# Kernel optimization log

Measured on AMD Instinct MI355X. Metric: run time of the kernel, lower is better.

Reference implementation:

```python
import jax, jax.numpy as jnp
import numpy as np
import math

B, H, T, N = 2, 4, 2048, 2048
THETA = 2.0 ** 16


def get_freqs(n: int, theta: float) -> jnp.ndarray:
    # quantize arange to multiples of 2, matching torch (t/2).floor()*2
    t = jnp.arange(n, dtype=jnp.float32)
    q = jnp.floor(t / 2.0) * 2.0
    return 1.0 / theta ** (q / n) / (2.0 * math.pi)


def rope(phases: jnp.ndarray, v: jnp.ndarray) -> jnp.ndarray:
    # v: [B,H,T,N]; phases: [T,N] (broadcast). Interleaved pair rotation.
    ph = (phases % 1.0) * (2.0 * math.pi)
    c, s = jnp.cos(ph), jnp.sin(ph)
    v2 = v.reshape(*v.shape[:-1], -1, 2)           # [...,N/2,2]
    v_rot = jnp.stack((-v2[..., 1], v2[..., 0]), axis=-1).reshape(v.shape)
    return (v * c + v_rot * s).astype(v.dtype)


def setup_inputs() -> dict:
    key = jax.random.key(0)
    kq, kv = jax.random.split(key)
    Q = jax.random.normal(kq, (B, H, T, N), dtype=jnp.float32)
    V = jax.random.normal(kv, (B, H, T, N), dtype=jnp.float32)
    return {"Q": Q, "V": V}


def reference(Q, V):
    Tlen = Q.shape[2]
    n = Q.shape[3]
    freqs = get_freqs(n, THETA)                               # [N]
    phases = jnp.arange(Tlen, dtype=jnp.float32)[:, None] * freqs[None, :]  # [T,N]
    QR = rope(phases, Q)                                      # K is Q -> KR = QR
    scores = jnp.einsum('bhtn,bhsn->bhts', QR, QR)            # [B,H,T,T]
    # strictly-causal mask: keep s < t (tril with diagonal=-1)
    mask = jnp.tril(jnp.ones((Tlen, Tlen), dtype=bool), k=-1)
    scores = jnp.where(mask, scores, 0.0)
    out = jnp.einsum('bhts,bhsn->bhtn', scores, V)
    return out
```

## Files before the change

kernel.cpp:

```cpp
#include <hip/hip_runtime.h>
#include <hip/hip_bf16.h>

#define TDIM 2048
#define NDIM 2048
#define BHN  8
#define LD   2048

typedef __attribute__((ext_vector_type(8))) short bf16x8;
typedef __attribute__((ext_vector_type(4))) float f32x4;
typedef unsigned short us;

static __device__ __forceinline__ us f2bf(float x) {
  union { __hip_bfloat16 h; us u; } cv;
  cv.h = __float2bfloat16(x);
  return cv.u;
}

__global__ __launch_bounds__(256) void rope_kernel(const float* __restrict__ Q,
                                                   us* __restrict__ QR,
                                                   int total8) {
  int idx = blockIdx.x * blockDim.x + threadIdx.x;
  if (idx >= total8) return;
  long base = (long)idx * 8;
  int n = (int)(base & (NDIM - 1));
  int t = (int)((base >> 11) & (TDIM - 1));
  const float4* p = reinterpret_cast<const float4*>(Q + base);
  float4 v0 = p[0], v1 = p[1];
  float q[8] = {v0.x, v0.y, v0.z, v0.w, v1.x, v1.y, v1.z, v1.w};
  us r[8];
  float tf = (float)t;
#pragma unroll
  for (int pr = 0; pr < 4; ++pr) {
    int nn = n + pr * 2;
    float freq = __builtin_exp2f((float)nn * (-1.0f / 128.0f)) * 0.15915494309189535f;
    float ph = tf * freq;
    ph = ph - __builtin_floorf(ph);
    float c = __builtin_amdgcn_cosf(ph);
    float s = __builtin_amdgcn_sinf(ph);
    float e = q[2 * pr], o = q[2 * pr + 1];
    r[2 * pr]     = f2bf(e * c - o * s);
    r[2 * pr + 1] = f2bf(o * c + e * s);
  }
  union { us usv[8]; bf16x8 v; } pk;
#pragma unroll
  for (int i = 0; i < 8; ++i) pk.usv[i] = r[i];
  *reinterpret_cast<bf16x8*>(QR + base) = pk.v;
}

__global__ __launch_bounds__(256) void vtrans_kernel(const float* __restrict__ V,
                                                     us* __restrict__ VT,
                                                     us* __restrict__ Sflag) {
  __shared__ float tile[32][33];
  if (Sflag != nullptr && blockIdx.x == 0 && blockIdx.y == 0 && blockIdx.z == 0 &&
      threadIdx.x == 0 && threadIdx.y == 0) {
    for (int h = 0; h < BHN; ++h) {
      unsigned* f = (unsigned*)(Sflag + (long)h * TDIM * LD + 1792);
      for (int i = 0; i < 40; ++i)
        __hip_atomic_store(&f[i], 0u, __ATOMIC_RELAXED, __HIP_MEMORY_SCOPE_AGENT);
    }
  }
  int bh = blockIdx.z;
  int n0 = blockIdx.x * 32, t0 = blockIdx.y * 32;
  const float* Vp = V + (long)bh * TDIM * NDIM;
  us* Tp = VT + (long)bh * TDIM * NDIM;
  int tx = threadIdx.x, ty = threadIdx.y;
#pragma unroll
  for (int i = 0; i < 4; ++i)
    tile[ty + i * 8][tx] = Vp[(long)(t0 + ty + i * 8) * NDIM + n0 + tx];
  __syncthreads();
#pragma unroll
  for (int i = 0; i < 4; ++i)
    Tp[(long)(n0 + ty + i * 8) * TDIM + t0 + tx] = f2bf(tile[tx][ty + i * 8]);
}

template <int PASS>
__device__ __forceinline__ void run_tile(const us* __restrict__ A,
                                         const us* __restrict__ B,
                                         void* __restrict__ Cbase,
                                         us* __restrict__ lds,
                                         int rt, int ct, int tid,
                                         unsigned* __restrict__ fh) {
  const int lane = tid & 63, wid = tid >> 6;
  const int wr = wid >> 2, wc = wid & 3;
  const int l15 = lane & 15, l4 = lane >> 4;
  const int row0 = rt * 256, col0 = ct * 256;
  const int kts = (PASS == 0) ? 32 : (rt + 1) * 4;
  const int fbase = rt * (rt + 1) / 2;

  if constexpr (PASS == 1) {
    if (wid == 0) {
      unsigned need = (1u << (rt + 1)) - 1u;
      for (;;) {
        unsigned ok = 0;
        if (lane <= rt)
          ok = (__hip_atomic_fetch_add(&fh[fbase + lane], 0u, __ATOMIC_RELAXED,
                                       __HIP_MEMORY_SCOPE_AGENT) != 0u);
        unsigned long long m = __ballot(ok);
        if (((unsigned)m & need) == need) break;
        __builtin_amdgcn_s_sleep(8);
      }
    }
    __builtin_amdgcn_s_barrier();
    asm volatile("" ::: "memory");
  }

  f32x4 acc[8][4];
#pragma unroll
  for (int m = 0; m < 8; ++m)
#pragma unroll
    for (int n = 0; n < 4; ++n) acc[m][n] = (f32x4){0.f, 0.f, 0.f, 0.f};

  auto stage = [&](int half , int t) {
    const us* g0 = (half < 2) ? A : B;
    const int tr0 = (half < 2) ? row0 : col0;
    const int h = half & 1;
    us* lb = lds + ((half < 2) ? 0 : 32768) + (t & 1) * 16384;
    const int k0 = t * 64;
#pragma unroll
    for (int r = 0; r < 2; ++r) {
      int off = r * 512 + tid;
      int row = off >> 3;
      int ch = off & 7;
      int chl = ch ^ (row & 7);
      const us* g = g0 + (long)(tr0 + h * 128 + row) * LD + (k0 + chl * 8);
      us* l = lb + h * 8192 + off * 8;
      __builtin_amdgcn_global_load_lds(
          (const __attribute__((address_space(1))) unsigned int*)g,
          (__attribute__((address_space(3))) unsigned int*)l, 16, 0, 0);
    }
  };
  auto ldA = [&](int b, int m, int ks) -> bf16x8 {
    int row = wr * 128 + m * 16 + l15;
    int ch = (ks * 4 + l4) ^ (row & 7);
    return *reinterpret_cast<const bf16x8*>(lds + b * 16384 + row * 64 + ch * 8);
  };
  auto ldB = [&](int b, int n, int ks) -> bf16x8 {
    int row = wc * 64 + n * 16 + l15;
    int ch = (ks * 4 + l4) ^ (row & 7);
    return *reinterpret_cast<const bf16x8*>(lds + 32768 + b * 16384 + row * 64 + ch * 8);
  };

  stage(0, 0); stage(1, 0); stage(2, 0); stage(3, 0);
  if (1 < kts) { stage(2, 1); stage(3, 1); }
  asm volatile("s_waitcnt vmcnt(4)" ::: "memory");
  __builtin_amdgcn_s_barrier();
  __builtin_amdgcn_sched_barrier(0);

  bf16x8 af[4][2], bfr[4][2];
  for (int t = 0; t < kts; ++t) {
    const int b = t & 1;
#pragma unroll
    for (int m = 0; m < 4; ++m) { af[m][0] = ldA(b, m, 0); af[m][1] = ldA(b, m, 1); }
#pragma unroll
    for (int n = 0; n < 2; ++n) { bfr[n][0] = ldB(b, n, 0); bfr[n][1] = ldB(b, n, 1); }
    if (t + 1 < kts) stage(0, t + 1);
    __builtin_amdgcn_s_barrier();
    asm volatile("s_waitcnt lgkmcnt(0)" ::: "memory");
    __builtin_amdgcn_sched_barrier(0);
    __builtin_amdgcn_s_setprio(1);
#pragma unroll
    for (int m = 0; m < 4; ++m)
#pragma unroll
      for (int n = 0; n < 2; ++n)
#pragma unroll
        for (int ks = 0; ks < 2; ++ks)
          acc[m][n] = __builtin_amdgcn_mfma_f32_16x16x32_bf16(af[m][ks], bfr[n][ks], acc[m][n], 0, 0, 0);
    __builtin_amdgcn_s_setprio(0);
    __builtin_amdgcn_sched_barrier(0);
    __builtin_amdgcn_s_barrier();
#pragma unroll
    for (int n = 2; n < 4; ++n) { bfr[n][0] = ldB(b, n, 0); bfr[n][1] = ldB(b, n, 1); }
    if (t + 1 < kts) stage(1, t + 1);
    __builtin_amdgcn_s_barrier();
    asm volatile("s_waitcnt lgkmcnt(0)" ::: "memory");
    __builtin_amdgcn_sched_barrier(0);
    __builtin_amdgcn_s_setprio(1);
#pragma unroll
    for (int m = 0; m < 4; ++m)
#pragma unroll
      for (int n = 2; n < 4; ++n)
#pragma unroll
        for (int ks = 0; ks < 2; ++ks)
          acc[m][n] = __builtin_amdgcn_mfma_f32_16x16x32_bf16(af[m][ks], bfr[n][ks], acc[m][n], 0, 0, 0);
    __builtin_amdgcn_s_setprio(0);
    __builtin_amdgcn_sched_barrier(0);
    __builtin_amdgcn_s_barrier();
#pragma unroll
    for (int m = 0; m < 4; ++m) { af[m][0] = ldA(b, m + 4, 0); af[m][1] = ldA(b, m + 4, 1); }
    if (t + 2 < kts) stage(2, t + 2);
    __builtin_amdgcn_s_barrier();
    asm volatile("s_waitcnt lgkmcnt(0)" ::: "memory");
    __builtin_amdgcn_sched_barrier(0);
    __builtin_amdgcn_s_setprio(1);
#pragma unroll
    for (int m = 0; m < 4; ++m)
#pragma unroll
      for (int n = 0; n < 2; ++n)
#pragma unroll
        for (int ks = 0; ks < 2; ++ks)
          acc[m + 4][n] = __builtin_amdgcn_mfma_f32_16x16x32_bf16(af[m][ks], bfr[n][ks], acc[m + 4][n], 0, 0, 0);
    __builtin_amdgcn_s_setprio(0);
    __builtin_amdgcn_sched_barrier(0);
    __builtin_amdgcn_s_barrier();
    if (t + 2 < kts) stage(3, t + 2);
    __builtin_amdgcn_s_setprio(1);
#pragma unroll
    for (int m = 0; m < 4; ++m)
#pragma unroll
      for (int n = 2; n < 4; ++n)
#pragma unroll
        for (int ks = 0; ks < 2; ++ks)
          acc[m + 4][n] = __builtin_amdgcn_mfma_f32_16x16x32_bf16(af[m][ks], bfr[n][ks], acc[m + 4][n], 0, 0, 0);
    __builtin_amdgcn_s_setprio(0);
    if (t + 2 < kts) { asm volatile("s_waitcnt vmcnt(4)" ::: "memory"); }
    else             { asm volatile("s_waitcnt vmcnt(0)" ::: "memory"); }
    __builtin_amdgcn_sched_barrier(0);
    __builtin_amdgcn_s_barrier();
    __builtin_amdgcn_sched_barrier(0);
  }

  if constexpr (PASS == 0) {
    us* C = (us*)Cbase;
    const bool diag = (rt == ct);
#pragma unroll
    for (int m = 0; m < 8; ++m) {
      int r0 = row0 + wr * 128 + m * 16 + l4 * 4;
#pragma unroll
      for (int n = 0; n < 4; ++n) {
        int cc = col0 + wc * 64 + n * 16 + l15;
#pragma unroll
        for (int j = 0; j < 4; ++j) {
          int tt = r0 + j;
          float v = acc[m][n][j];
          if (diag && cc >= tt) v = 0.0f;
          C[(long)tt * LD + cc] = f2bf(v);
        }
      }
    }
    __syncthreads();
    if (tid == 0)
      __hip_atomic_store(&fh[fbase + ct], 1u, __ATOMIC_RELEASE,
                         __HIP_MEMORY_SCOPE_AGENT);
  } else {
    float* C = (float*)Cbase;
#pragma unroll
    for (int m = 0; m < 8; ++m) {
      int r0 = row0 + wr * 128 + m * 16 + l4 * 4;
#pragma unroll
      for (int n = 0; n < 4; ++n) {
        int cc = col0 + wc * 64 + n * 16 + l15;
#pragma unroll
        for (int j = 0; j < 4; ++j)
          __builtin_nontemporal_store(acc[m][n][j], &C[(long)(r0 + j) * LD + cc]);
      }
    }
  }
}

__global__ __launch_bounds__(512, 2) void gemm_fused(const us* __restrict__ QR,
                                                     const us* __restrict__ VT,
                                                     us* __restrict__ S,
                                                     float* __restrict__ Out) {
  extern __shared__ us lds[];
  const int b = (int)blockIdx.x;
  const int head = b & 7, u = b >> 3;
  const int tid = (int)threadIdx.x;
  const us* QRh = QR + (long)head * TDIM * LD;
  const us* VTh = VT + (long)head * TDIM * LD;
  us* Sh = S + (long)head * TDIM * LD;
  float* Oh = Out + (long)head * TDIM * LD;
  unsigned* fh = (unsigned*)(Sh + 1792);
  unsigned* qc = fh + 36;

  int rt0, ct0;
  if (u < 8)       { rt0 = 7; ct0 = u; }
  else if (u < 15) { rt0 = 6; ct0 = u - 8; }
  else if (u < 21) { rt0 = 5; ct0 = u - 15; }
  else if (u < 26) { rt0 = 4; ct0 = u - 21; }
  else if (u < 30) { rt0 = 3; ct0 = u - 26; }
  else             { rt0 = 2; ct0 = (u == 30) ? 0 : 2; }
  run_tile<0>(QRh, QRh, Sh, lds, rt0, ct0, tid, fh);
  if (u >= 28) {
    int rt1, ct1;
    if (u == 28)      { rt1 = 1; ct1 = 0; }
    else if (u == 29) { rt1 = 1; ct1 = 1; }
    else if (u == 30) { rt1 = 2; ct1 = 1; }
    else              { rt1 = 0; ct1 = 0; }
    run_tile<0>(QRh, QRh, Sh, lds, rt1, ct1, tid, fh);
    run_tile<1>(Sh, VTh, Oh, lds, 1, u - 28, tid, fh);
  }

  for (;;) {
    if (tid == 0) {
      unsigned i = __hip_atomic_fetch_add(qc, 1u, __ATOMIC_RELAXED,
                                          __HIP_MEMORY_SCOPE_AGENT);
      *(volatile unsigned*)lds = i;
    }
    __syncthreads();
    unsigned i = *(volatile unsigned*)lds;
    __syncthreads();
    if (i >= 60) break;
    int rt, ct;
    if (i < 48)      { rt = 7 - (int)(i >> 3); ct = (int)(i & 7); }
    else if (i < 52) { rt = 1; ct = (int)(i - 44); }
    else             { rt = 0; ct = (int)(i - 52); }
    run_tile<1>(Sh, VTh, Oh, lds, rt, ct, tid, fh);
  }
}

template <int PASS>
__global__ __launch_bounds__(512, 2) void gemm256(
    const us* __restrict__ Abase, const us* __restrict__ Bbase,
    void* __restrict__ Cbase, int nh) {
  extern __shared__ us lds[];
  int bid = (int)blockIdx.x;
  int head, rt = 0, ct, cls = 0;
  if constexpr (PASS == 0) {
    head = bid % nh;
    int tri = bid / nh;
    rt = 0;
    while ((rt + 1) * (rt + 2) / 2 <= tri) ++rt;
    ct = tri - rt * (rt + 1) / 2;
  } else {
    head = bid % nh;
    int rem = bid / nh;
    ct = rem & 7;
    cls = rem >> 3;
  }
  const us* A = Abase + (long)head * TDIM * LD;
  const us* B = Bbase + (long)head * TDIM * LD;
  us* Sh = (us*)Cbase + (long)head * TDIM * LD;
  const int tid = (int)threadIdx.x;
  const int NSEG = (PASS == 0) ? 1 : 2;
#pragma unroll 1
  for (int seg = 0; seg < NSEG; ++seg) {
    int rts = rt, cts = ct;
    if constexpr (PASS == 1) { rts = seg ? cls : 7 - cls; cts = ct; }
    if constexpr (PASS == 0) {
      run_tile<0>(A, A, Sh, lds, rts, cts, tid, (unsigned*)(Sh + 1792));
    } else {
      float* Oh = (float*)Cbase + (long)head * TDIM * LD;
      run_tile<1>(A, B, Oh, lds, rts, cts, tid,
                  (unsigned*)((us*)Abase + (long)head * TDIM * LD + 1792));
    }
  }
}

extern "C" void kernel_launch(void* const* d_in, const int* in_sizes, int n_in,
                              void* d_out, int out_size, void* d_ws, size_t ws_size,
                              hipStream_t stream) {
  const float* Q = (const float*)d_in[0];
  const float* V = (const float*)d_in[1];
  float* Out = (float*)d_out;
  char* ws = (char*)d_ws;
  const long TN = (long)TDIM * NDIM;
  const size_t BUF = (size_t)BHN * TN * 2;
  const size_t PERBH = (size_t)TN * 2;
  const int SHMEM = 131072;

  hipFuncSetAttribute(reinterpret_cast<const void*>(&gemm_fused),
                      hipFuncAttributeMaxDynamicSharedMemorySize, SHMEM);
  hipFuncSetAttribute(reinterpret_cast<const void*>(&gemm256<0>),
                      hipFuncAttributeMaxDynamicSharedMemorySize, SHMEM);
  hipFuncSetAttribute(reinterpret_cast<const void*>(&gemm256<1>),
                      hipFuncAttributeMaxDynamicSharedMemorySize, SHMEM);

  if (ws_size >= 3 * BUF) {
    us* QRb = (us*)ws;
    us* VbT = (us*)(ws + BUF);
    us* S   = (us*)(ws + 2 * BUF);
    int total8 = (int)(BHN * TN / 8);
    rope_kernel<<<dim3(total8 / 256), dim3(256), 0, stream>>>(Q, QRb, total8);
    vtrans_kernel<<<dim3(64, 64, 8), dim3(32, 8), 0, stream>>>(V, VbT, S);
    void* args[] = {(void*)&QRb, (void*)&VbT, (void*)&S, (void*)&Out};
    hipError_t ce = hipLaunchCooperativeKernel(
        reinterpret_cast<const void*>(&gemm_fused), dim3(256), dim3(512),
        args, (unsigned)SHMEM, stream);
    if (ce != hipSuccess) {
      (void)hipGetLastError();
      gemm256<0><<<dim3(36 * BHN), dim3(512), SHMEM, stream>>>(QRb, QRb, S, BHN);
      gemm256<1><<<dim3(32 * BHN), dim3(512), SHMEM, stream>>>(S, VbT, Out, BHN);
    }
  } else {
    us* QR0 = (us*)ws;
    us* VT0 = (us*)(ws + PERBH);
    us* S0  = (us*)(ws + 2 * PERBH);
    int total8 = (int)(TN / 8);
    for (int bh = 0; bh < BHN; ++bh) {
      rope_kernel<<<dim3(total8 / 256), dim3(256), 0, stream>>>(Q + bh * TN, QR0, total8);
      vtrans_kernel<<<dim3(64, 64, 1), dim3(32, 8), 0, stream>>>(V + bh * TN, VT0, S0);
      gemm256<0><<<dim3(36), dim3(512), SHMEM, stream>>>(QR0, QR0, S0, 1);
      gemm256<1><<<dim3(32), dim3(512), SHMEM, stream>>>(S0, VT0, Out + bh * TN, 1);
    }
  }
}
```

Measured before the change: 259.0 us.

## Widen V transpose tiles, prefetch B before flag wait, unroll k-loop by two

The V transpose kernel now moves 64x64 tiles, loading float4 per thread and storing packed bf16 quads, which reduces the number of global transactions. In the second GEMM pass the B-operand (V^T) tile loads are issued before spinning on the readiness flags, so their latency overlaps the wait. The k-loop is unrolled by two with the LDS buffer index made a compile-time constant, which simplifies addressing. Output stores switch from nontemporal to ordinary stores, which changes cache behaviour for the large fp32 output.

```diff
diff --git a/kernel.cpp b/kernel.cpp
--- a/kernel.cpp
+++ b/kernel.cpp
@@ -9,6 +9,8 @@
 typedef __attribute__((ext_vector_type(8))) short bf16x8;
 typedef __attribute__((ext_vector_type(4))) float f32x4;
 typedef unsigned short us;
+
+template <int N> struct ic { static constexpr int v = N; };
 
 static __device__ __forceinline__ us f2bf(float x) {
   union { __hip_bfloat16 h; us u; } cv;
@@ -50,27 +52,47 @@
 __global__ __launch_bounds__(256) void vtrans_kernel(const float* __restrict__ V,
                                                      us* __restrict__ VT,
                                                      us* __restrict__ Sflag) {
-  __shared__ float tile[32][33];
+  __shared__ float tile[64 * 66];
   if (Sflag != nullptr && blockIdx.x == 0 && blockIdx.y == 0 && blockIdx.z == 0 &&
-      threadIdx.x == 0 && threadIdx.y == 0) {
+      threadIdx.x == 0) {
     for (int h = 0; h < BHN; ++h) {
       unsigned* f = (unsigned*)(Sflag + (long)h * TDIM * LD + 1792);
       for (int i = 0; i < 40; ++i)
         __hip_atomic_store(&f[i], 0u, __ATOMIC_RELAXED, __HIP_MEMORY_SCOPE_AGENT);
     }
   }
-  int bh = blockIdx.z;
-  int n0 = blockIdx.x * 32, t0 = blockIdx.y * 32;
+  const int bh = blockIdx.z;
+  const int t0 = blockIdx.x * 64, n0 = blockIdx.y * 64;
   const float* Vp = V + (long)bh * TDIM * NDIM;
   us* Tp = VT + (long)bh * TDIM * NDIM;
-  int tx = threadIdx.x, ty = threadIdx.y;
-#pragma unroll
-  for (int i = 0; i < 4; ++i)
-    tile[ty + i * 8][tx] = Vp[(long)(t0 + ty + i * 8) * NDIM + n0 + tx];
+  const int tid = (int)threadIdx.x;
+  {
+    const int tx4 = tid & 15, ty = tid >> 4;
+#pragma unroll
+    for (int i = 0; i < 4; ++i) {
+      int row = ty + i * 16;
+      float4 v = *reinterpret_cast<const float4*>(
+          Vp + (long)(t0 + row) * NDIM + n0 + tx4 * 4);
+      float* d = &tile[row * 66 + tx4 * 4];
+      d[0] = v.x; d[1] = v.y; d[2] = v.z; d[3] = v.w;
+    }
+  }
   __syncthreads();
-#pragma unroll
-  for (int i = 0; i < 4; ++i)
-    Tp[(long)(n0 + ty + i * 8) * TDIM + t0 + tx] = f2bf(tile[tx][ty + i * 8]);
+  {
+    const int sx = tid & 15, sy = tid >> 4;
+#pragma unroll
+    for (int j = 0; j < 4; ++j) {
+      int n = sy * 4 + j;
+      unsigned r0 = f2bf(tile[(sx * 4 + 0) * 66 + n]);
+      unsigned r1 = f2bf(tile[(sx * 4 + 1) * 66 + n]);
+      unsigned r2 = f2bf(tile[(sx * 4 + 2) * 66 + n]);
+      unsigned r3 = f2bf(tile[(sx * 4 + 3) * 66 + n]);
+      uint2 val;
+      val.x = r0 | (r1 << 16);
+      val.y = r2 | (r3 << 16);
+      *reinterpret_cast<uint2*>(Tp + (long)(n0 + n) * TDIM + t0 + sx * 4) = val;
+    }
+  }
 }
 
 template <int PASS>
@@ -87,7 +109,44 @@
   const int kts = (PASS == 0) ? 32 : (rt + 1) * 4;
   const int fbase = rt * (rt + 1) / 2;
 
+  f32x4 acc[8][4];
+#pragma unroll
+  for (int m = 0; m < 8; ++m)
+#pragma unroll
+    for (int n = 0; n < 4; ++n) acc[m][n] = (f32x4){0.f, 0.f, 0.f, 0.f};
+
+  auto stage = [&](int half , int t) {
+    const us* g0 = (half < 2) ? A : B;
+    const int tr0 = (half < 2) ? row0 : col0;
+    const int h = half & 1;
+    us* lb = lds + ((half < 2) ? 0 : 32768) + (t & 1) * 16384;
+    const int k0 = t * 64;
+#pragma unroll
+    for (int r = 0; r < 2; ++r) {
+      int off = r * 512 + tid;
+      int row = off >> 3;
+      int ch = off & 7;
+      int chl = ch ^ (row & 7);
+      const us* g = g0 + (long)(tr0 + h * 128 + row) * LD + (k0 + chl * 8);
+      us* l = lb + h * 8192 + off * 8;
+      __builtin_amdgcn_global_load_lds(
+          (const __attribute__((address_space(1))) unsigned int*)g,
+          (__attribute__((address_space(3))) unsigned int*)l, 16, 0, 0);
+    }
+  };
+  auto ldA = [&](int b, int m, int ks) -> bf16x8 {
+    int row = wr * 128 + m * 16 + l15;
+    int ch = (ks * 4 + l4) ^ (row & 7);
+    return *reinterpret_cast<const bf16x8*>(lds + b * 16384 + row * 64 + ch * 8);
+  };
+  auto ldB = [&](int b, int n, int ks) -> bf16x8 {
+    int row = wc * 64 + n * 16 + l15;
+    int ch = (ks * 4 + l4) ^ (row & 7);
+    return *reinterpret_cast<const bf16x8*>(lds + 32768 + b * 16384 + row * 64 + ch * 8);
+  };
+
   if constexpr (PASS == 1) {
+    stage(2, 0); stage(3, 0);
     if (wid == 0) {
       unsigned need = (1u << (rt + 1)) - 1u;
       for (;;) {
@@ -102,53 +161,19 @@
     }
     __builtin_amdgcn_s_barrier();
     asm volatile("" ::: "memory");
-  }
-
-  f32x4 acc[8][4];
-#pragma unroll
-  for (int m = 0; m < 8; ++m)
-#pragma unroll
-    for (int n = 0; n < 4; ++n) acc[m][n] = (f32x4){0.f, 0.f, 0.f, 0.f};
-
-  auto stage = [&](int half , int t) {
-    const us* g0 = (half < 2) ? A : B;
-    const int tr0 = (half < 2) ? row0 : col0;
-    const int h = half & 1;
-    us* lb = lds + ((half < 2) ? 0 : 32768) + (t & 1) * 16384;
-    const int k0 = t * 64;
-#pragma unroll
-    for (int r = 0; r < 2; ++r) {
-      int off = r * 512 + tid;
-      int row = off >> 3;
-      int ch = off & 7;
-      int chl = ch ^ (row & 7);
-      const us* g = g0 + (long)(tr0 + h * 128 + row) * LD + (k0 + chl * 8);
-      us* l = lb + h * 8192 + off * 8;
-      __builtin_amdgcn_global_load_lds(
-          (const __attribute__((address_space(1))) unsigned int*)g,
-          (__attribute__((address_space(3))) unsigned int*)l, 16, 0, 0);
-    }
-  };
-  auto ldA = [&](int b, int m, int ks) -> bf16x8 {
-    int row = wr * 128 + m * 16 + l15;
-    int ch = (ks * 4 + l4) ^ (row & 7);
-    return *reinterpret_cast<const bf16x8*>(lds + b * 16384 + row * 64 + ch * 8);
-  };
-  auto ldB = [&](int b, int n, int ks) -> bf16x8 {
-    int row = wc * 64 + n * 16 + l15;
-    int ch = (ks * 4 + l4) ^ (row & 7);
-    return *reinterpret_cast<const bf16x8*>(lds + 32768 + b * 16384 + row * 64 + ch * 8);
-  };
-
-  stage(0, 0); stage(1, 0); stage(2, 0); stage(3, 0);
-  if (1 < kts) { stage(2, 1); stage(3, 1); }
+    stage(0, 0); stage(1, 0);
+    if (1 < kts) { stage(2, 1); stage(3, 1); }
+  } else {
+    stage(0, 0); stage(1, 0); stage(2, 0); stage(3, 0);
+    if (1 < kts) { stage(2, 1); stage(3, 1); }
+  }
   asm volatile("s_waitcnt vmcnt(4)" ::: "memory");
   __builtin_amdgcn_s_barrier();
   __builtin_amdgcn_sched_barrier(0);
 
   bf16x8 af[4][2], bfr[4][2];
-  for (int t = 0; t < kts; ++t) {
-    const int b = t & 1;
+  auto kstep = [&](int t, auto bbc) {
+    constexpr int b = decltype(bbc)::v;
 #pragma unroll
     for (int m = 0; m < 4; ++m) { af[m][0] = ldA(b, m, 0); af[m][1] = ldA(b, m, 1); }
 #pragma unroll
@@ -217,6 +242,10 @@
     __builtin_amdgcn_sched_barrier(0);
     __builtin_amdgcn_s_barrier();
     __builtin_amdgcn_sched_barrier(0);
+  };
+  for (int t = 0; t < kts; t += 2) {
+    kstep(t, ic<0>{});
+    kstep(t + 1, ic<1>{});
   }
 
   if constexpr (PASS == 0) {
@@ -251,7 +280,7 @@
         int cc = col0 + wc * 64 + n * 16 + l15;
 #pragma unroll
         for (int j = 0; j < 4; ++j)
-          __builtin_nontemporal_store(acc[m][n][j], &C[(long)(r0 + j) * LD + cc]);
+          C[(long)(r0 + j) * LD + cc] = acc[m][n][j];
       }
     }
   }
@@ -371,7 +400,7 @@
     us* S   = (us*)(ws + 2 * BUF);
     int total8 = (int)(BHN * TN / 8);
     rope_kernel<<<dim3(total8 / 256), dim3(256), 0, stream>>>(Q, QRb, total8);
-    vtrans_kernel<<<dim3(64, 64, 8), dim3(32, 8), 0, stream>>>(V, VbT, S);
+    vtrans_kernel<<<dim3(32, 32, 8), dim3(256), 0, stream>>>(V, VbT, S);
     void* args[] = {(void*)&QRb, (void*)&VbT, (void*)&S, (void*)&Out};
     hipError_t ce = hipLaunchCooperativeKernel(
         reinterpret_cast<const void*>(&gemm_fused), dim3(256), dim3(512),
@@ -388,7 +417,7 @@
     int total8 = (int)(TN / 8);
     for (int bh = 0; bh < BHN; ++bh) {
       rope_kernel<<<dim3(total8 / 256), dim3(256), 0, stream>>>(Q + bh * TN, QR0, total8);
-      vtrans_kernel<<<dim3(64, 64, 1), dim3(32, 8), 0, stream>>>(V + bh * TN, VT0, S0);
+      vtrans_kernel<<<dim3(32, 32, 1), dim3(256), 0, stream>>>(V + bh * TN, VT0, S0);
       gemm256<0><<<dim3(36), dim3(512), SHMEM, stream>>>(QR0, QR0, S0, 1);
       gemm256<1><<<dim3(32), dim3(512), SHMEM, stream>>>(S0, VT0, Out + bh * TN, 1);
     }
```

Measured after the change: 280.2 us. +8.2%, slower.
